# Kernel optimization log

Hardware: AMD Instinct MI355X
Metric: run time of the kernel (lower is better)

Reference implementation:

```python
import jax, jax.numpy as jnp
import numpy as np

NUM_LEAVES = 256
EPS = 1e-6
SHARPNESS = 1.0   # init_sharpness, non-trainable buffer
BIAS_SHIFT = -2.0


def _generalized_gcd(w1, w2, lambd):
    # lambd: per-node bias -> andness via sigmoid; broadcast over batch
    lam = jax.nn.sigmoid(lambd)
    a = jnp.abs(w1) + EPS
    b = jnp.abs(w2) + EPS
    return lam * jnp.minimum(a, b) + (1.0 - lam) * jnp.maximum(a, b)


def setup_inputs() -> dict:
    key = jax.random.key(0)
    ks = jax.random.split(key, 6)
    B, L = 65536, NUM_LEAVES
    x = jax.random.normal(ks[0], (B, L), jnp.float32)
    # xavier-like scale for the leaf projection
    W_leaf = jax.random.normal(ks[1], (L, L), jnp.float32) * (1.0 / np.sqrt(L))
    weights = jax.random.uniform(ks[2], (L - 1, 2), jnp.float32, 0.5, 1.5)
    biases = jax.random.uniform(ks[3], (L - 1,), jnp.float32) * 0.1
    w_out = jax.random.normal(ks[4], (1, 1), jnp.float32)
    b_out = jnp.full((1,), 0.5, jnp.float32)
    return {"x": x, "W_leaf": W_leaf, "weights": weights,
            "biases": biases, "w_out": w_out, "b_out": b_out}


def reference(x, W_leaf, weights, biases, w_out, b_out):
    # InputToLeafFC: sigmoid(sharpness * (x @ W^T + bias_shift))
    leaf = jax.nn.sigmoid(SHARPNESS * (x @ W_leaf.T + BIAS_SHIFT))  # (B, L)

    # The original pops two nodes from the front of the queue and appends the
    # result; for a power-of-two leaf count this is exactly a level-by-level
    # pairwise tree reduction, with node weights consumed in order.
    cur = leaf
    off = 0
    n = cur.shape[1]
    while n > 1:  # log2(L) levels, each fully vectorized over (batch, pairs)
        m = n // 2
        w = weights[off:off + m]   # (m, 2)
        b = biases[off:off + m]    # (m,)
        left = cur[:, 0::2] * w[:, 0]
        right = cur[:, 1::2] * w[:, 1]
        cur = _generalized_gcd(left, right, b)  # (B, m)
        off += m
        n = m
    # fc_out: Linear(1,1) then sigmoid -> (B, 1)
    return jax.nn.sigmoid(cur * w_out[0, 0] + b_out[0])
```

## Files before the change

### kernel.cpp

```cpp
#include <hip/hip_runtime.h>
#include <stdint.h>


#define EPS 1e-6f
#define LOG2E 1.44269504088896340736f
#define WSTR 264
#define WIMG_SHORTS (256 * WSTR)

typedef __attribute__((ext_vector_type(8))) short short8;
typedef __attribute__((ext_vector_type(4))) short short4_t;
typedef __attribute__((ext_vector_type(4))) float float4_t;

__device__ __forceinline__ float fast_sigmoid(float z) {
    float e = __builtin_amdgcn_exp2f(-z * LOG2E);
    return __builtin_amdgcn_rcpf(1.0f + e);
}

__device__ __forceinline__ short f2bf(float f) {
    uint32_t u = __builtin_bit_cast(uint32_t, f);
    u += 0x7FFFu + ((u >> 16) & 1u);
    return (short)(u >> 16);
}

__device__ __forceinline__ float ggcd(float l, float r, float lam) {
    float a = fabsf(l) + EPS;
    float b = fabsf(r) + EPS;
    float mn = fminf(a, b);
    float mx = fmaxf(a, b);
    return fmaf(lam, mn - mx, mx);
}

__device__ __forceinline__ void tree_reduce(float4_t acc[16], int c0,
                                            const float4* pv, float res[4]) {
    #pragma unroll
    for (int t = 0; t < 16; ++t) {
        #pragma unroll
        for (int r = 0; r < 4; ++r) acc[t][r] = fast_sigmoid(acc[t][r] - 2.0f);
    }
    #pragma unroll
    for (int tp = 0; tp < 8; ++tp) {
        float4 p = pv[c0 * 8 + tp];
        #pragma unroll
        for (int r = 0; r < 4; ++r)
            acc[tp][r] = ggcd(acc[2*tp][r] * p.x, acc[2*tp+1][r] * p.y, p.z);
    }
    #pragma unroll
    for (int tp = 0; tp < 4; ++tp) {
        float4 p = pv[128 + c0 * 4 + tp];
        #pragma unroll
        for (int r = 0; r < 4; ++r)
            acc[tp][r] = ggcd(acc[2*tp][r] * p.x, acc[2*tp+1][r] * p.y, p.z);
    }
    #pragma unroll
    for (int tp = 0; tp < 2; ++tp) {
        float4 p = pv[192 + c0 * 2 + tp];
        #pragma unroll
        for (int r = 0; r < 4; ++r)
            acc[tp][r] = ggcd(acc[2*tp][r] * p.x, acc[2*tp+1][r] * p.y, p.z);
    }
    {
        float4 p = pv[224 + c0];
        #pragma unroll
        for (int r = 0; r < 4; ++r)
            res[r] = ggcd(acc[0][r] * p.x, acc[1][r] * p.y, p.z);
    }
}

__global__ __launch_bounds__(512, 2)
void btln_fused(const float* __restrict__ x, const float* __restrict__ Wl,
                const float* __restrict__ wts, const float* __restrict__ bia,
                const float* __restrict__ wout, const float* __restrict__ bout,
                float* __restrict__ out) {
    __shared__ short Ws[WIMG_SHORTS];
    __shared__ float4 pv[256];

    const int tid  = threadIdx.x;
    const int lane = tid & 63;
    const int wv   = tid >> 6;
    const int c0   = lane & 15;
    const int q    = lane >> 4;

    {
        const float4* Wv4 = (const float4*)Wl;
        #pragma unroll 4
        for (int it = 0; it < 32; ++it) {
            int i   = it * 512 + tid;
            int j   = i >> 6;
            int kc4 = i & 63;
            float4 w4 = Wv4[i];
            int p = ((j & 15) << 4) | (j >> 4);
            short4_t s4;
            s4.x = f2bf(w4.x); s4.y = f2bf(w4.y); s4.z = f2bf(w4.z); s4.w = f2bf(w4.w);
            *(short4_t*)&Ws[p * WSTR + kc4 * 4] = s4;
        }
    }
    if (tid < 255)
        pv[tid] = make_float4(wts[2 * tid], wts[2 * tid + 1], fast_sigmoid(bia[tid]), 0.f);
    __syncthreads();

    const int rowbase = blockIdx.x * 256 + wv * 32;
    const float4* xv0 = (const float4*)(x + (size_t)(rowbase + c0) * 256);
    const float4* xv1 = (const float4*)(x + (size_t)(rowbase + 16 + c0) * 256);

    float4_t acc0[16], acc1[16];
    #pragma unroll
    for (int t = 0; t < 16; ++t) {
        acc0[t] = (float4_t){0.f, 0.f, 0.f, 0.f};
        acc1[t] = (float4_t){0.f, 0.f, 0.f, 0.f};
    }

    float4 a00 = xv0[q * 2], a01 = xv0[q * 2 + 1];
    float4 a10 = xv1[q * 2], a11 = xv1[q * 2 + 1];
    #pragma unroll 1
    for (int kt = 0; kt < 8; ++kt) {
        const int ktn = (kt < 7) ? kt + 1 : 7;
        float4 n00 = xv0[ktn * 8 + q * 2], n01 = xv0[ktn * 8 + q * 2 + 1];
        float4 n10 = xv1[ktn * 8 + q * 2], n11 = xv1[ktn * 8 + q * 2 + 1];

        short8 af0, af1;
        af0[0] = f2bf(a00.x); af0[1] = f2bf(a00.y); af0[2] = f2bf(a00.z); af0[3] = f2bf(a00.w);
        af0[4] = f2bf(a01.x); af0[5] = f2bf(a01.y); af0[6] = f2bf(a01.z); af0[7] = f2bf(a01.w);
        af1[0] = f2bf(a10.x); af1[1] = f2bf(a10.y); af1[2] = f2bf(a10.z); af1[3] = f2bf(a10.w);
        af1[4] = f2bf(a11.x); af1[5] = f2bf(a11.y); af1[6] = f2bf(a11.z); af1[7] = f2bf(a11.w);

        const int kk = kt * 32;
        #pragma unroll
        for (int t = 0; t < 16; ++t) {
            short8 bf = *(const short8*)&Ws[(t * 16 + c0) * WSTR + kk + q * 8];
            acc0[t] = __builtin_amdgcn_mfma_f32_16x16x32_bf16(af0, bf, acc0[t], 0, 0, 0);
            acc1[t] = __builtin_amdgcn_mfma_f32_16x16x32_bf16(af1, bf, acc1[t], 0, 0, 0);
        }
        a00 = n00; a01 = n01; a10 = n10; a11 = n11;
    }

    float res0[4], res1[4];
    tree_reduce(acc0, c0, pv, res0);
    tree_reduce(acc1, c0, pv, res1);

    const int offs[4] = {240, 248, 252, 254};
    #pragma unroll
    for (int k = 0; k < 4; ++k) {
        float4 p = pv[offs[k] + (c0 >> (k + 1))];
        bool isLeft = ((c0 >> k) & 1) == 0;
        #pragma unroll
        for (int r = 0; r < 4; ++r) {
            float o0 = __shfl_xor(res0[r], 1 << k, 64);
            float o1 = __shfl_xor(res1[r], 1 << k, 64);
            float lf0 = isLeft ? res0[r] : o0, rt0 = isLeft ? o0 : res0[r];
            float lf1 = isLeft ? res1[r] : o1, rt1 = isLeft ? o1 : res1[r];
            res0[r] = ggcd(lf0 * p.x, rt0 * p.y, p.z);
            res1[r] = ggcd(lf1 * p.x, rt1 * p.y, p.z);
        }
    }

    if (c0 == 0) {
        const float wo = wout[0];
        const float bo = bout[0];
        #pragma unroll
        for (int r = 0; r < 4; ++r) {
            out[rowbase + q * 4 + r]      = fast_sigmoid(fmaf(res0[r], wo, bo));
            out[rowbase + 16 + q * 4 + r] = fast_sigmoid(fmaf(res1[r], wo, bo));
        }
    }
}

extern "C" void kernel_launch(void* const* d_in, const int* in_sizes, int n_in,
                              void* d_out, int out_size, void* d_ws, size_t ws_size,
                              hipStream_t stream) {
    const float* x   = (const float*)d_in[0];
    const float* Wl  = (const float*)d_in[1];
    const float* wts = (const float*)d_in[2];
    const float* bia = (const float*)d_in[3];
    const float* wo  = (const float*)d_in[4];
    const float* bo  = (const float*)d_in[5];
    float* out = (float*)d_out;

    const int rows = out_size;
    dim3 grid(rows / 256), block(512);
    btln_fused<<<grid, block, 0, stream>>>(x, Wl, wts, bia, wo, bo, out);
}
```

Baseline: 115.7 us.

## Load x coalesced up front and transpose via per-wave LDS strips

Each wave now loads its 32 rows of x with row-contiguous coalesced float4 loads at kernel start, before the W staging. It converts them to bf16 in registers, then for each k-tile writes one band into a small per-wave LDS strip and reads it back in MFMA fragment layout. This replaces the per-lane strided row reads and the one-tile-ahead register prefetch. The aim is more bytes in flight and better coalescing, with the x load overlapping the W image build. The cost is 64 extra VGPRs for the packed x, with spill or occupancy risk under the 512x2 launch bounds, plus extra LDS traffic per tile.

```diff
diff --git a/kernel.cpp b/kernel.cpp
--- a/kernel.cpp
+++ b/kernel.cpp
@@ -6,10 +6,12 @@
 #define LOG2E 1.44269504088896340736f
 #define WSTR 264
 #define WIMG_SHORTS (256 * WSTR)
+#define XSTR 144
 
 typedef __attribute__((ext_vector_type(8))) short short8;
 typedef __attribute__((ext_vector_type(4))) short short4_t;
 typedef __attribute__((ext_vector_type(4))) float float4_t;
+typedef __attribute__((ext_vector_type(4))) unsigned int uint4_t;
 
 __device__ __forceinline__ float fast_sigmoid(float z) {
     float e = __builtin_amdgcn_exp2f(-z * LOG2E);
@@ -20,6 +22,13 @@
     uint32_t u = __builtin_bit_cast(uint32_t, f);
     u += 0x7FFFu + ((u >> 16) & 1u);
     return (short)(u >> 16);
+}
+
+__device__ __forceinline__ short8 pack8(float4 a, float4 b) {
+    short8 s;
+    s[0] = f2bf(a.x); s[1] = f2bf(a.y); s[2] = f2bf(a.z); s[3] = f2bf(a.w);
+    s[4] = f2bf(b.x); s[5] = f2bf(b.y); s[6] = f2bf(b.z); s[7] = f2bf(b.w);
+    return s;
 }
 
 __device__ __forceinline__ float ggcd(float l, float r, float lam) {
@@ -73,12 +82,31 @@
                 float* __restrict__ out) {
     __shared__ short Ws[WIMG_SHORTS];
     __shared__ float4 pv[256];
+    __shared__ char Xs[8 * 2 * 8 * XSTR];
 
     const int tid  = threadIdx.x;
     const int lane = tid & 63;
     const int wv   = tid >> 6;
     const int c0   = lane & 15;
     const int q    = lane >> 4;
+    const int band = lane >> 3;
+    const int jj   = lane & 7;
+
+    const int rowbase = blockIdx.x * 256 + wv * 32;
+
+    const float4* xb = (const float4*)(x + (size_t)rowbase * 256);
+    short8 C8[16];
+    {
+        float4 R[16];
+        #pragma unroll
+        for (int i = 0; i < 16; ++i) R[i] = xb[i * 64 + lane];
+        #pragma unroll
+        for (int i = 0; i < 8; ++i) C8[i] = pack8(R[2*i], R[2*i+1]);
+        #pragma unroll
+        for (int i = 0; i < 16; ++i) R[i] = xb[(16 + i) * 64 + lane];
+        #pragma unroll
+        for (int i = 0; i < 8; ++i) C8[8 + i] = pack8(R[2*i], R[2*i+1]);
+    }
 
     {
         const float4* Wv4 = (const float4*)Wl;
@@ -98,9 +126,8 @@
         pv[tid] = make_float4(wts[2 * tid], wts[2 * tid + 1], fast_sigmoid(bia[tid]), 0.f);
     __syncthreads();
 
-    const int rowbase = blockIdx.x * 256 + wv * 32;
-    const float4* xv0 = (const float4*)(x + (size_t)(rowbase + c0) * 256);
-    const float4* xv1 = (const float4*)(x + (size_t)(rowbase + 16 + c0) * 256);
+    char* strip0 = &Xs[wv * (2 * 8 * XSTR)];
+    char* strip1 = strip0 + 8 * XSTR;
 
     float4_t acc0[16], acc1[16];
     #pragma unroll
@@ -109,19 +136,27 @@
         acc1[t] = (float4_t){0.f, 0.f, 0.f, 0.f};
     }
 
-    float4 a00 = xv0[q * 2], a01 = xv0[q * 2 + 1];
-    float4 a10 = xv1[q * 2], a11 = xv1[q * 2 + 1];
     #pragma unroll 1
     for (int kt = 0; kt < 8; ++kt) {
-        const int ktn = (kt < 7) ? kt + 1 : 7;
-        float4 n00 = xv0[ktn * 8 + q * 2], n01 = xv0[ktn * 8 + q * 2 + 1];
-        float4 n10 = xv1[ktn * 8 + q * 2], n11 = xv1[ktn * 8 + q * 2 + 1];
-
-        short8 af0, af1;
-        af0[0] = f2bf(a00.x); af0[1] = f2bf(a00.y); af0[2] = f2bf(a00.z); af0[3] = f2bf(a00.w);
-        af0[4] = f2bf(a01.x); af0[5] = f2bf(a01.y); af0[6] = f2bf(a01.z); af0[7] = f2bf(a01.w);
-        af1[0] = f2bf(a10.x); af1[1] = f2bf(a10.y); af1[2] = f2bf(a10.z); af1[3] = f2bf(a10.w);
-        af1[4] = f2bf(a11.x); af1[5] = f2bf(a11.y); af1[6] = f2bf(a11.z); af1[7] = f2bf(a11.w);
+        if (band == kt) {
+            char* s0 = strip0 + jj * XSTR;
+            char* s1 = strip1 + jj * XSTR;
+            #pragma unroll
+            for (int i = 0; i < 8; ++i) {
+                *(short8*)(s0 + i * 16) = C8[i];
+                *(short8*)(s1 + i * 16) = C8[8 + i];
+            }
+        }
+        asm volatile("" ::: "memory");
+        const char* r0 = strip0 + (2 * q) * XSTR + c0 * 8;
+        const char* r1 = strip1 + (2 * q) * XSTR + c0 * 8;
+        uint2 lo0 = *(const uint2*)r0;
+        uint2 hi0 = *(const uint2*)(r0 + XSTR);
+        uint2 lo1 = *(const uint2*)r1;
+        uint2 hi1 = *(const uint2*)(r1 + XSTR);
+        asm volatile("" ::: "memory");
+        short8 af0 = __builtin_bit_cast(short8, (uint4_t){lo0.x, lo0.y, hi0.x, hi0.y});
+        short8 af1 = __builtin_bit_cast(short8, (uint4_t){lo1.x, lo1.y, hi1.x, hi1.y});
 
         const int kk = kt * 32;
         #pragma unroll
@@ -130,7 +165,6 @@
             acc0[t] = __builtin_amdgcn_mfma_f32_16x16x32_bf16(af0, bf, acc0[t], 0, 0, 0);
             acc1[t] = __builtin_amdgcn_mfma_f32_16x16x32_bf16(af1, bf, acc1[t], 0, 0, 0);
         }
-        a00 = n00; a01 = n01; a10 = n10; a11 = n11;
     }
 
     float res0[4], res1[4];
```

New measurement: 122.1 us. +5.6%, slower.
